# Optimization experiments

Measured on AMD Instinct MI355X. Metric: run time of the kernel, lower is better.

## Reference

```python
import jax, jax.numpy as jnp
import numpy as np

B, N, M, BUCKETS = 4096, 2048, 2048, 16
T = 100.0  # softmax temperature from module (self.T = 100)


def _make_values(buckets):
    b = buckets // 2
    v = np.zeros((buckets, 1), np.float32)
    for i in range(buckets):
        v[i, 0] = 1.0 / 2.0 ** (b - i) if i < b else -1.0 / 2.0 ** (i - b)
    return jnp.asarray(v)


def setup_inputs() -> dict:
    key = jax.random.key(0)
    ks = jax.random.split(key, 7)
    scale = 1.0 / np.sqrt(M)  # nn.Linear default init range
    return {
        "x": jax.random.normal(ks[0], (B, M), jnp.float32),
        "x_hash": jax.random.normal(ks[1], (B, M), jnp.float32),
        "weight": jax.random.uniform(ks[2], (N, M), jnp.float32, -scale, scale),
        "bias": jax.random.uniform(ks[3], (N,), jnp.float32, -scale, scale),
        "a0": jax.random.normal(ks[4], (BUCKETS, 1), jnp.float32),
        "a1": jax.random.normal(ks[5], (BUCKETS, 1), jnp.float32),
        "a2": jax.random.normal(ks[6], (BUCKETS, 1), jnp.float32),
        "values": _make_values(BUCKETS),
    }


def reference(x, x_hash, weight, bias, a0, a1, a2, values):
    n, m = weight.shape
    fcw = weight.reshape(1, -1)                       # [1, N*M]
    # rank-1 outer products + bias: fx [buckets, N*M]
    fx = a1 @ fcw + a2 @ (fcw * fcw) + a0
    probs = jax.nn.softmax(fx * T, axis=0)            # softmax over buckets
    hash_weight = (probs.T @ values).reshape(n, m)    # [N, M]
    out = x @ weight.T + bias                         # [B, N]
    out_hash = x_hash @ hash_weight.T + bias          # [B, N]
    return out, out_hash
```

## Files before the change

### kernel.cpp

```cpp
#include <hip/hip_runtime.h>
#include <hip/hip_bf16.h>

typedef __attribute__((ext_vector_type(8))) short bf16x8;
typedef __attribute__((ext_vector_type(4))) float f32x4;
typedef __attribute__((ext_vector_type(8))) unsigned short u16x8;
typedef __attribute__((ext_vector_type(4))) unsigned short u16x4;

__device__ __forceinline__ unsigned short f2bf_rtne(float f) {
    unsigned int u = __float_as_uint(f);
    u += 0x7FFFu + ((u >> 16) & 1u);
    return (unsigned short)(u >> 16);
}

__device__ __forceinline__ void gl2lds16(const void* g, void* l) {
    __builtin_amdgcn_global_load_lds((const __attribute__((address_space(1))) void*)g,
                                     (__attribute__((address_space(3))) void*)l, 16, 0, 0);
}

#define NB 16
__global__ void prep_all(const float* __restrict__ x, const float* __restrict__ xh,
                         const float* __restrict__ w,
                         const float* __restrict__ a0, const float* __restrict__ a1,
                         const float* __restrict__ a2, const float* __restrict__ vals,
                         unsigned short* __restrict__ xb, unsigned short* __restrict__ xhb,
                         unsigned short* __restrict__ wbf, unsigned short* __restrict__ hwbf) {
    const int job = blockIdx.y;
    const int stride = gridDim.x * blockDim.x;
    int i = blockIdx.x * blockDim.x + threadIdx.x;
    if (job < 2) {
        const float* in = job ? xh : x;
        unsigned short* out = job ? xhb : xb;
        const int n8 = (4096 * 2048) / 8;
        for (; i < n8; i += stride) {
            const float4* p = (const float4*)in + (size_t)i * 2;
            float4 v0 = p[0];
            float4 v1 = p[1];
            u16x8 r;
            r[0] = f2bf_rtne(v0.x); r[1] = f2bf_rtne(v0.y); r[2] = f2bf_rtne(v0.z); r[3] = f2bf_rtne(v0.w);
            r[4] = f2bf_rtne(v1.x); r[5] = f2bf_rtne(v1.y); r[6] = f2bf_rtne(v1.z); r[7] = f2bf_rtne(v1.w);
            *((u16x8*)out + i) = r;
        }
    } else {
        float A0[NB], A1[NB], A2[NB], V[NB];
#pragma unroll
        for (int b = 0; b < NB; ++b) {
            A0[b] = a0[b] * 100.0f;
            A1[b] = a1[b] * 100.0f;
            A2[b] = a2[b] * 100.0f;
            V[b]  = vals[b];
        }
        const int n4 = (2048 * 2048) / 4;
        for (; i < n4; i += stride) {
            float4 wv = ((const float4*)w)[i];
            float win[4] = {wv.x, wv.y, wv.z, wv.w};
            u16x4 wr, hr;
#pragma unroll
            for (int c = 0; c < 4; ++c) {
                float xx = win[c];
                float x2 = xx * xx;
                float l[NB];
                float mx = -1e30f;
#pragma unroll
                for (int b = 0; b < NB; ++b) {
                    l[b] = fmaf(A1[b], xx, fmaf(A2[b], x2, A0[b]));
                    mx = fmaxf(mx, l[b]);
                }
                float s = 0.0f, acc = 0.0f;
#pragma unroll
                for (int b = 0; b < NB; ++b) {
                    float e = __expf(l[b] - mx);
                    s += e;
                    acc = fmaf(e, V[b], acc);
                }
                wr[c] = f2bf_rtne(xx);
                hr[c] = f2bf_rtne(acc / s);
            }
            *((u16x4*)wbf + i)  = wr;
            *((u16x4*)hwbf + i) = hr;
        }
    }
}

__global__ __launch_bounds__(512, 2) void gemm256(
    const unsigned short* __restrict__ Ax, const unsigned short* __restrict__ Ah,
    const unsigned short* __restrict__ Bw, const unsigned short* __restrict__ Bh,
    const float* __restrict__ bias,
    float* __restrict__ Cx, float* __restrict__ Chh) {
    const int K = 2048, N = 2048;

    __shared__ unsigned short lds[65536];

    const unsigned short* A  = blockIdx.z ? Ah : Ax;
    const unsigned short* Bm = blockIdx.z ? Bh : Bw;
    float* C = blockIdx.z ? Chh : Cx;

    const int tid  = threadIdx.x;
    const int lane = tid & 63;
    const int wid  = tid >> 6;
    const int wr = wid >> 2;
    const int wc = wid & 3;
    const int fr = lane & 15;
    const int fq = lane >> 4;
    const int brow = blockIdx.x;
    const int bcol = blockIdx.y;

    const int srow = tid >> 3;
    const int sg8  = ((tid & 7) ^ (srow & 7)) * 8;
    const unsigned short* gA = A  + (size_t)(brow * 256 + srow) * K + sg8;
    const unsigned short* gB = Bm + (size_t)(bcol * 256 + srow) * K + sg8;
    const int wbase = wid * 512;

    const int g0 = (fq ^ (fr & 7)) * 8;
    const int g1 = g0 ^ 32;

#define STAGE_A(buf, h, j) {                                                    \
    const unsigned short* _g = gA + (size_t)((h) * 128) * K + (j) * 64;         \
    gl2lds16(_g,                  lds + (buf) * 16384 + (h) * 8192 + wbase);    \
    gl2lds16(_g + (size_t)64 * K, lds + (buf) * 16384 + (h) * 8192 + 4096 + wbase); }
#define STAGE_B(buf, h, j) {                                                    \
    const unsigned short* _g = gB + (size_t)((h) * 128) * K + (j) * 64;         \
    gl2lds16(_g,                  lds + 32768 + (buf) * 16384 + (h) * 8192 + wbase); \
    gl2lds16(_g + (size_t)64 * K, lds + 32768 + (buf) * 16384 + (h) * 8192 + 4096 + wbase); }

#define RDA(dst, buf, mblk) {                                                   \
    const unsigned short* _p = lds + (buf) * 16384 + (wr * 128 + (mblk) * 16 + fr) * 64; \
    dst[0] = *(const bf16x8*)(_p + g0);                                         \
    dst[1] = *(const bf16x8*)(_p + g1); }
#define RDB(dst, buf, nblk) {                                                   \
    const unsigned short* _p = lds + 32768 + (buf) * 16384 + (wc * 64 + (nblk) * 16 + fr) * 64; \
    dst[0] = *(const bf16x8*)(_p + g0);                                         \
    dst[1] = *(const bf16x8*)(_p + g1); }
#define RD_BURST(buf) { RDB(bfr[0], buf, 0); RDB(bfr[1], buf, 1);               \
                        RDB(bfr[2], buf, 2); RDB(bfr[3], buf, 3); }

#define MM(mi, n, kk, AF) acc[mi][n] = __builtin_amdgcn_mfma_f32_16x16x32_bf16(AF[kk], bfr[n][kk], acc[mi][n], 0, 0, 0)

#define PH(q, A0_, A1_, RDS, STG, TAILP) {                                      \
    __builtin_amdgcn_s_barrier();                                               \
    asm volatile("" ::: "memory");                                              \
    RDS;                                                                        \
    STG;                                                                        \
    __builtin_amdgcn_s_setprio(1);                                              \
    MM(2*(q),0,0,A0_); MM(2*(q),0,1,A0_); MM(2*(q)+1,0,0,A1_); MM(2*(q)+1,0,1,A1_); \
    MM(2*(q),1,0,A0_); MM(2*(q),1,1,A0_); MM(2*(q)+1,1,0,A1_); MM(2*(q)+1,1,1,A1_); \
    MM(2*(q),2,0,A0_); MM(2*(q),2,1,A0_); MM(2*(q)+1,2,0,A1_); MM(2*(q)+1,2,1,A1_); \
    MM(2*(q),3,0,A0_); MM(2*(q),3,1,A0_); MM(2*(q)+1,3,0,A1_); MM(2*(q)+1,3,1,A1_); \
    __builtin_amdgcn_s_setprio(0);                                              \
    TAILP;                                                                      \
    asm volatile("" ::: "memory"); }

#define GATE4 { asm volatile("s_waitcnt vmcnt(4)" ::: "memory");                \
                __builtin_amdgcn_s_barrier(); }
#define GATE0 { asm volatile("s_waitcnt vmcnt(0)" ::: "memory");                \
                __builtin_amdgcn_s_barrier(); }

    STAGE_A(0, 0, 0); STAGE_A(0, 1, 0);
    STAGE_B(0, 0, 0); STAGE_B(0, 1, 0);
    STAGE_B(1, 0, 1); STAGE_B(1, 1, 1);
    asm volatile("s_waitcnt vmcnt(4)" ::: "memory");

    f32x4 acc[8][4] = {};
    bf16x8 bfr[4][2], aU0[2], aU1[2], aV0[2], aV1[2];

#pragma unroll 1
    for (int t = 0; t < 15; ++t) {
        const int j1 = 2 * t + 1, j2 = 2 * t + 2, j3 = 2 * t + 3;
        PH(0, aU0, aU1, { RD_BURST(0); RDA(aU0,0,0); RDA(aU1,0,1); RDA(aV0,0,2); RDA(aV1,0,3); },
           STAGE_A(1, 0, j1), );
        PH(1, aV0, aV1, { RDA(aU0,0,4); RDA(aU1,0,5); }, STAGE_A(1, 1, j1), );
        PH(2, aU0, aU1, { RDA(aV0,0,6); RDA(aV1,0,7); }, STAGE_B(0, 0, j2), );
        PH(3, aV0, aV1, , STAGE_B(0, 1, j2), GATE4);
        PH(0, aU0, aU1, { RD_BURST(1); RDA(aU0,1,0); RDA(aU1,1,1); RDA(aV0,1,2); RDA(aV1,1,3); },
           STAGE_A(0, 0, j2), );
        PH(1, aV0, aV1, { RDA(aU0,1,4); RDA(aU1,1,5); }, STAGE_A(0, 1, j2), );
        PH(2, aU0, aU1, { RDA(aV0,1,6); RDA(aV1,1,7); }, STAGE_B(1, 0, j3), );
        PH(3, aV0, aV1, , STAGE_B(1, 1, j3), GATE4);
    }
    PH(0, aU0, aU1, { RD_BURST(0); RDA(aU0,0,0); RDA(aU1,0,1); RDA(aV0,0,2); RDA(aV1,0,3); },
       STAGE_A(1, 0, 31), );
    PH(1, aV0, aV1, { RDA(aU0,0,4); RDA(aU1,0,5); }, STAGE_A(1, 1, 31), );
    PH(2, aU0, aU1, { RDA(aV0,0,6); RDA(aV1,0,7); }, , );
    PH(3, aV0, aV1, , , GATE0);
    PH(0, aU0, aU1, { RD_BURST(1); RDA(aU0,1,0); RDA(aU1,1,1); RDA(aV0,1,2); RDA(aV1,1,3); }, , );
    PH(1, aV0, aV1, { RDA(aU0,1,4); RDA(aU1,1,5); }, , );
    PH(2, aU0, aU1, { RDA(aV0,1,6); RDA(aV1,1,7); }, , );
    PH(3, aV0, aV1, , , );

#pragma unroll
    for (int n = 0; n < 4; ++n) {
        const int col = bcol * 256 + wc * 64 + n * 16 + fr;
        const float bv = bias[col];
#pragma unroll
        for (int m = 0; m < 8; ++m) {
            const int row0 = brow * 256 + wr * 128 + m * 16 + fq * 4;
#pragma unroll
            for (int r = 0; r < 4; ++r)
                C[(size_t)(row0 + r) * N + col] = acc[m][n][r] + bv;
        }
    }
#undef STAGE_A
#undef STAGE_B
#undef RDA
#undef RDB
#undef RD_BURST
#undef MM
#undef PH
#undef GATE4
#undef GATE0
}

extern "C" void kernel_launch(void* const* d_in, const int* in_sizes, int n_in,
                              void* d_out, int out_size, void* d_ws, size_t ws_size,
                              hipStream_t stream) {
    const float* x    = (const float*)d_in[0];
    const float* xh   = (const float*)d_in[1];
    const float* w    = (const float*)d_in[2];
    const float* bias = (const float*)d_in[3];
    const float* a0   = (const float*)d_in[4];
    const float* a1   = (const float*)d_in[5];
    const float* a2   = (const float*)d_in[6];
    const float* vals = (const float*)d_in[7];

    float* out  = (float*)d_out;
    float* outh = out + (size_t)4096 * 2048;

    char* ws = (char*)d_ws;
    unsigned short* xb  = (unsigned short*)(ws);
    unsigned short* xhb = (unsigned short*)(ws + (size_t)16 * 1024 * 1024);
    unsigned short* wb  = (unsigned short*)(ws + (size_t)32 * 1024 * 1024);
    unsigned short* hwb = (unsigned short*)(ws + (size_t)40 * 1024 * 1024);

    prep_all<<<dim3(2048, 3), 256, 0, stream>>>(x, xh, w, a0, a1, a2, vals, xb, xhb, wb, hwb);

    dim3 grid(4096 / 256, 2048 / 256, 2);
    gemm256<<<grid, 512, 0, stream>>>(xb, xhb, wb, hwb, bias, out, outh);
}
```

Baseline: 98.17 us.

## Fuse fp32-to-bf16 activation conversion into GEMM A-tile staging

```diff
diff --git a/kernel.cpp b/kernel.cpp
--- a/kernel.cpp
+++ b/kernel.cpp
@@ -18,71 +18,52 @@
 }
 
 #define NB 16
-__global__ void prep_all(const float* __restrict__ x, const float* __restrict__ xh,
-                         const float* __restrict__ w,
-                         const float* __restrict__ a0, const float* __restrict__ a1,
-                         const float* __restrict__ a2, const float* __restrict__ vals,
-                         unsigned short* __restrict__ xb, unsigned short* __restrict__ xhb,
-                         unsigned short* __restrict__ wbf, unsigned short* __restrict__ hwbf) {
-    const int job = blockIdx.y;
+__global__ void hash_prep(const float* __restrict__ w,
+                          const float* __restrict__ a0, const float* __restrict__ a1,
+                          const float* __restrict__ a2, const float* __restrict__ vals,
+                          unsigned short* __restrict__ wbf, unsigned short* __restrict__ hwbf) {
+    float A0[NB], A1[NB], A2[NB], V[NB];
+#pragma unroll
+    for (int b = 0; b < NB; ++b) {
+        A0[b] = a0[b] * 100.0f;
+        A1[b] = a1[b] * 100.0f;
+        A2[b] = a2[b] * 100.0f;
+        V[b]  = vals[b];
+    }
+    const int n4 = (2048 * 2048) / 4;
     const int stride = gridDim.x * blockDim.x;
-    int i = blockIdx.x * blockDim.x + threadIdx.x;
-    if (job < 2) {
-        const float* in = job ? xh : x;
-        unsigned short* out = job ? xhb : xb;
-        const int n8 = (4096 * 2048) / 8;
-        for (; i < n8; i += stride) {
-            const float4* p = (const float4*)in + (size_t)i * 2;
-            float4 v0 = p[0];
-            float4 v1 = p[1];
-            u16x8 r;
-            r[0] = f2bf_rtne(v0.x); r[1] = f2bf_rtne(v0.y); r[2] = f2bf_rtne(v0.z); r[3] = f2bf_rtne(v0.w);
-            r[4] = f2bf_rtne(v1.x); r[5] = f2bf_rtne(v1.y); r[6] = f2bf_rtne(v1.z); r[7] = f2bf_rtne(v1.w);
-            *((u16x8*)out + i) = r;
+    for (int i = blockIdx.x * blockDim.x + threadIdx.x; i < n4; i += stride) {
+        float4 wv = ((const float4*)w)[i];
+        float win[4] = {wv.x, wv.y, wv.z, wv.w};
+        u16x4 wr, hr;
+#pragma unroll
+        for (int c = 0; c < 4; ++c) {
+            float xx = win[c];
+            float x2 = xx * xx;
+            float l[NB];
+            float mx = -1e30f;
+#pragma unroll
+            for (int b = 0; b < NB; ++b) {
+                l[b] = fmaf(A1[b], xx, fmaf(A2[b], x2, A0[b]));
+                mx = fmaxf(mx, l[b]);
+            }
+            float s = 0.0f, acc = 0.0f;
+#pragma unroll
+            for (int b = 0; b < NB; ++b) {
+                float e = __expf(l[b] - mx);
+                s += e;
+                acc = fmaf(e, V[b], acc);
+            }
+            wr[c] = f2bf_rtne(xx);
+            hr[c] = f2bf_rtne(acc / s);
         }
-    } else {
-        float A0[NB], A1[NB], A2[NB], V[NB];
-#pragma unroll
-        for (int b = 0; b < NB; ++b) {
-            A0[b] = a0[b] * 100.0f;
-            A1[b] = a1[b] * 100.0f;
-            A2[b] = a2[b] * 100.0f;
-            V[b]  = vals[b];
-        }
-        const int n4 = (2048 * 2048) / 4;
-        for (; i < n4; i += stride) {
-            float4 wv = ((const float4*)w)[i];
-            float win[4] = {wv.x, wv.y, wv.z, wv.w};
-            u16x4 wr, hr;
-#pragma unroll
-            for (int c = 0; c < 4; ++c) {
-                float xx = win[c];
-                float x2 = xx * xx;
-                float l[NB];
-                float mx = -1e30f;
-#pragma unroll
-                for (int b = 0; b < NB; ++b) {
-                    l[b] = fmaf(A1[b], xx, fmaf(A2[b], x2, A0[b]));
-                    mx = fmaxf(mx, l[b]);
-                }
-                float s = 0.0f, acc = 0.0f;
-#pragma unroll
-                for (int b = 0; b < NB; ++b) {
-                    float e = __expf(l[b] - mx);
-                    s += e;
-                    acc = fmaf(e, V[b], acc);
-                }
-                wr[c] = f2bf_rtne(xx);
-                hr[c] = f2bf_rtne(acc / s);
-            }
-            *((u16x4*)wbf + i)  = wr;
-            *((u16x4*)hwbf + i) = hr;
-        }
+        *((u16x4*)wbf + i)  = wr;
+        *((u16x4*)hwbf + i) = hr;
     }
 }
 
 __global__ __launch_bounds__(512, 2) void gemm256(
-    const unsigned short* __restrict__ Ax, const unsigned short* __restrict__ Ah,
+    const float* __restrict__ Axf, const float* __restrict__ Ahf,
     const unsigned short* __restrict__ Bw, const unsigned short* __restrict__ Bh,
     const float* __restrict__ bias,
     float* __restrict__ Cx, float* __restrict__ Chh) {
@@ -90,7 +71,7 @@
 
     __shared__ unsigned short lds[65536];
 
-    const unsigned short* A  = blockIdx.z ? Ah : Ax;
+    const float* Af = blockIdx.z ? Ahf : Axf;
     const unsigned short* Bm = blockIdx.z ? Bh : Bw;
     float* C = blockIdx.z ? Chh : Cx;
 
@@ -105,18 +86,40 @@
     const int bcol = blockIdx.y;
 
     const int srow = tid >> 3;
-    const int sg8  = ((tid & 7) ^ (srow & 7)) * 8;
-    const unsigned short* gA = A  + (size_t)(brow * 256 + srow) * K + sg8;
-    const unsigned short* gB = Bm + (size_t)(bcol * 256 + srow) * K + sg8;
+    const int aswz = ((tid & 7) ^ (srow & 7)) * 8;
+    const float* gAf = Af + (size_t)(brow * 256 + srow) * K + (tid & 7) * 8;
+    const unsigned short* gB = Bm + (size_t)(bcol * 256 + srow) * K + aswz;
     const int wbase = wid * 512;
 
     const int g0 = (fq ^ (fr & 7)) * 8;
     const int g1 = g0 ^ 32;
 
-#define STAGE_A(buf, h, j) {                                                    \
-    const unsigned short* _g = gA + (size_t)((h) * 128) * K + (j) * 64;         \
-    gl2lds16(_g,                  lds + (buf) * 16384 + (h) * 8192 + wbase);    \
-    gl2lds16(_g + (size_t)64 * K, lds + (buf) * 16384 + (h) * 8192 + 4096 + wbase); }
+#define LOAD_H0(R, j) {                                                         \
+    const float* _p = gAf + (size_t)(j) * 64;                                   \
+    R[0] = *(const float4*)(_p);                                                \
+    R[1] = *(const float4*)(_p + 4);                                            \
+    R[2] = *(const float4*)(_p + (size_t)64 * K);                               \
+    R[3] = *(const float4*)(_p + (size_t)64 * K + 4); }
+#define LOAD_H1(R, j) {                                                         \
+    const float* _p = gAf + (size_t)(j) * 64 + (size_t)128 * K;                 \
+    R[4] = *(const float4*)(_p);                                                \
+    R[5] = *(const float4*)(_p + 4);                                            \
+    R[6] = *(const float4*)(_p + (size_t)64 * K);                               \
+    R[7] = *(const float4*)(_p + (size_t)64 * K + 4); }
+#define CVT8(dst, a, b) {                                                       \
+    dst[0] = f2bf_rtne(a.x); dst[1] = f2bf_rtne(a.y);                           \
+    dst[2] = f2bf_rtne(a.z); dst[3] = f2bf_rtne(a.w);                           \
+    dst[4] = f2bf_rtne(b.x); dst[5] = f2bf_rtne(b.y);                           \
+    dst[6] = f2bf_rtne(b.z); dst[7] = f2bf_rtne(b.w); }
+#define WRITE_H0(R, buf) {                                                      \
+    unsigned short* _d = lds + (buf) * 16384 + srow * 64 + aswz;                \
+    u16x8 _v0, _v1; CVT8(_v0, R[0], R[1]); CVT8(_v1, R[2], R[3]);               \
+    *(u16x8*)_d = _v0; *(u16x8*)(_d + 4096) = _v1; }
+#define WRITE_H1(R, buf) {                                                      \
+    unsigned short* _d = lds + (buf) * 16384 + 8192 + srow * 64 + aswz;         \
+    u16x8 _v0, _v1; CVT8(_v0, R[4], R[5]); CVT8(_v1, R[6], R[7]);               \
+    *(u16x8*)_d = _v0; *(u16x8*)(_d + 4096) = _v1; }
+
 #define STAGE_B(buf, h, j) {                                                    \
     const unsigned short* _g = gB + (size_t)((h) * 128) * K + (j) * 64;         \
     gl2lds16(_g,                  lds + 32768 + (buf) * 16384 + (h) * 8192 + wbase); \
@@ -154,31 +157,39 @@
 #define GATE0 { asm volatile("s_waitcnt vmcnt(0)" ::: "memory");                \
                 __builtin_amdgcn_s_barrier(); }
 
-    STAGE_A(0, 0, 0); STAGE_A(0, 1, 0);
+    float4 sP[8], sQ[8];
+
+    LOAD_H0(sP, 0); LOAD_H1(sP, 0);
+    LOAD_H0(sQ, 1); LOAD_H1(sQ, 1);
     STAGE_B(0, 0, 0); STAGE_B(0, 1, 0);
     STAGE_B(1, 0, 1); STAGE_B(1, 1, 1);
+    WRITE_H0(sP, 0); WRITE_H1(sP, 0);
     asm volatile("s_waitcnt vmcnt(4)" ::: "memory");
+    asm volatile("s_waitcnt lgkmcnt(0)" ::: "memory");
+    __builtin_amdgcn_s_barrier();
 
     f32x4 acc[8][4] = {};
     bf16x8 bfr[4][2], aU0[2], aU1[2], aV0[2], aV1[2];
 
 #pragma unroll 1
     for (int t = 0; t < 15; ++t) {
-        const int j1 = 2 * t + 1, j2 = 2 * t + 2, j3 = 2 * t + 3;
+        const int j2 = 2 * t + 2, j3 = 2 * t + 3;
         PH(0, aU0, aU1, { RD_BURST(0); RDA(aU0,0,0); RDA(aU1,0,1); RDA(aV0,0,2); RDA(aV1,0,3); },
-           STAGE_A(1, 0, j1), );
-        PH(1, aV0, aV1, { RDA(aU0,0,4); RDA(aU1,0,5); }, STAGE_A(1, 1, j1), );
+           { WRITE_H0(sQ, 1); LOAD_H0(sP, j2); }, );
+        PH(1, aV0, aV1, { RDA(aU0,0,4); RDA(aU1,0,5); },
+           { WRITE_H1(sQ, 1); LOAD_H1(sP, j2); }, );
         PH(2, aU0, aU1, { RDA(aV0,0,6); RDA(aV1,0,7); }, STAGE_B(0, 0, j2), );
         PH(3, aV0, aV1, , STAGE_B(0, 1, j2), GATE4);
         PH(0, aU0, aU1, { RD_BURST(1); RDA(aU0,1,0); RDA(aU1,1,1); RDA(aV0,1,2); RDA(aV1,1,3); },
-           STAGE_A(0, 0, j2), );
-        PH(1, aV0, aV1, { RDA(aU0,1,4); RDA(aU1,1,5); }, STAGE_A(0, 1, j2), );
+           { WRITE_H0(sP, 0); LOAD_H0(sQ, j3); }, );
+        PH(1, aV0, aV1, { RDA(aU0,1,4); RDA(aU1,1,5); },
+           { WRITE_H1(sP, 0); LOAD_H1(sQ, j3); }, );
         PH(2, aU0, aU1, { RDA(aV0,1,6); RDA(aV1,1,7); }, STAGE_B(1, 0, j3), );
         PH(3, aV0, aV1, , STAGE_B(1, 1, j3), GATE4);
     }
     PH(0, aU0, aU1, { RD_BURST(0); RDA(aU0,0,0); RDA(aU1,0,1); RDA(aV0,0,2); RDA(aV1,0,3); },
-       STAGE_A(1, 0, 31), );
-    PH(1, aV0, aV1, { RDA(aU0,0,4); RDA(aU1,0,5); }, STAGE_A(1, 1, 31), );
+       WRITE_H0(sQ, 1), );
+    PH(1, aV0, aV1, { RDA(aU0,0,4); RDA(aU1,0,5); }, WRITE_H1(sQ, 1), );
     PH(2, aU0, aU1, { RDA(aV0,0,6); RDA(aV1,0,7); }, , );
     PH(3, aV0, aV1, , , GATE0);
     PH(0, aU0, aU1, { RD_BURST(1); RDA(aU0,1,0); RDA(aU1,1,1); RDA(aV0,1,2); RDA(aV1,1,3); }, , );
@@ -198,7 +209,11 @@
                 C[(size_t)(row0 + r) * N + col] = acc[m][n][r] + bv;
         }
     }
-#undef STAGE_A
+#undef LOAD_H0
+#undef LOAD_H1
+#undef CVT8
+#undef WRITE_H0
+#undef WRITE_H1
 #undef STAGE_B
 #undef RDA
 #undef RDB
@@ -225,13 +240,11 @@
     float* outh = out + (size_t)4096 * 2048;
 
     char* ws = (char*)d_ws;
-    unsigned short* xb  = (unsigned short*)(ws);
-    unsigned short* xhb = (unsigned short*)(ws + (size_t)16 * 1024 * 1024);
-    unsigned short* wb  = (unsigned short*)(ws + (size_t)32 * 1024 * 1024);
-    unsigned short* hwb = (unsigned short*)(ws + (size_t)40 * 1024 * 1024);
-
-    prep_all<<<dim3(2048, 3), 256, 0, stream>>>(x, xh, w, a0, a1, a2, vals, xb, xhb, wb, hwb);
+    unsigned short* wb  = (unsigned short*)(ws);
+    unsigned short* hwb = (unsigned short*)(ws + (size_t)8 * 1024 * 1024);
+
+    hash_prep<<<2048, 256, 0, stream>>>(w, a0, a1, a2, vals, wb, hwb);
 
     dim3 grid(4096 / 256, 2048 / 256, 2);
-    gemm256<<<grid, 512, 0, stream>>>(xb, xhb, wb, hwb, bias, out, outh);
-}
+    gemm256<<<grid, 512, 0, stream>>>(x, xh, wb, hwb, bias, out, outh);
+}
```

Result: slower. 124.9 us (+27.3%).
